# Performance work log

Hardware: AMD Instinct MI355X
Metric: run time of the kernel (lower is better)

Reference implementation:

```python
import jax, jax.numpy as jnp
import numpy as np

N_NODES = 50000
N_GRAPHS = 512


def _gcn_layer(x, src, dst, W, b):
    # DGL GraphConv, norm='both', allow_zero_in_degree=True
    n = x.shape[0]
    ones = jnp.ones(src.shape[0], x.dtype)
    deg_out = jnp.zeros(n, x.dtype).at[src].add(ones)
    deg_in = jnp.zeros(n, x.dtype).at[dst].add(ones)
    norm_out = jax.lax.rsqrt(jnp.maximum(deg_out, 1.0))
    norm_in = jax.lax.rsqrt(jnp.maximum(deg_in, 1.0))
    h = x * norm_out[:, None]
    agg = jax.ops.segment_sum(h[src], dst, num_segments=n)  # SpMM
    return (agg * norm_in[:, None]) @ W + b


def setup_inputs() -> dict:
    key = jax.random.key(0)
    ks = jax.random.split(key, 16)
    E = 800000
    inp = {
        'nid': jax.random.randint(ks[0], (N_NODES,), 0, 100000),
        'z': jax.random.randint(ks[1], (N_NODES,), 0, 1000),
        'src': jax.random.randint(ks[2], (E,), 0, N_NODES),
        'dst': jax.random.randint(ks[3], (E,), 0, N_NODES),
        'graph_id': jnp.sort(jax.random.randint(ks[4], (N_NODES,), 0, N_GRAPHS)),
        'init_embed': jax.random.normal(ks[5], (100000, 64), jnp.float32) * 0.1,
        'z_table': jax.random.normal(ks[6], (1000, 64), jnp.float32) * 0.1,
        'W0': jax.random.normal(ks[7], (128, 128), jnp.float32) * 0.1,
        'b0': jnp.zeros((128,), jnp.float32),
        'W1': jax.random.normal(ks[8], (128, 128), jnp.float32) * 0.1,
        'b1': jnp.zeros((128,), jnp.float32),
        'W2': jax.random.normal(ks[9], (128, 128), jnp.float32) * 0.1,
        'b2': jnp.zeros((128,), jnp.float32),
        'lin1_W': jax.random.normal(ks[10], (128, 128), jnp.float32) * 0.1,
        'lin1_b': jnp.zeros((128,), jnp.float32),
        'lin2_W': jax.random.normal(ks[11], (128, 200), jnp.float32) * 0.1,
        'lin2_b': jnp.zeros((200,), jnp.float32),
    }
    return inp


def reference(nid, z, src, dst, graph_id, init_embed, z_table, W0, b0, W1, b1, W2, b2, lin1_W, lin1_b, lin2_W, lin2_b):
    # node features: entity embedding lookup + structural label embedding, concat
    x = jnp.concatenate([init_embed[nid], z_table[z]], axis=1)  # [N, 128]
    # layers[:-1] with relu (dropout is identity in eval mode)
    x = jax.nn.relu(_gcn_layer(x, src, dst, W0, b0))
    x = jax.nn.relu(_gcn_layer(x, src, dst, W1, b1))
    x = _gcn_layer(x, src, dst, W2, b2)
    # SumPooling over subgraphs in the batch
    g = jax.ops.segment_sum(x, graph_id, num_segments=N_GRAPHS)  # [G, 128]
    h = jax.nn.relu(g @ lin1_W + lin1_b)
    return h @ lin2_W + lin2_b  # [G, num_rel]
```

## Files before the change

kernel.cpp:

```cpp
#include <hip/hip_runtime.h>
#include <hip/hip_bf16.h>


#define FEAT 128
#define NG 512
#define CH 128
#define NPMAX 12544
#define LDW 136

typedef __attribute__((ext_vector_type(8))) short bf16x8;
typedef __attribute__((ext_vector_type(4))) float f32x4;

__device__ __forceinline__ float bf2f(unsigned short u) {
    union { unsigned int i; float f; } v; v.i = ((unsigned int)u) << 16; return v.f;
}
__device__ __forceinline__ unsigned short f2bf(float f) {
    unsigned int u = __float_as_uint(f);
    return (unsigned short)((u + 0x7FFFu + ((u >> 16) & 1u)) >> 16);
}
__device__ __forceinline__ float lo16(unsigned u) { return __uint_as_float(u << 16); }
__device__ __forceinline__ float hi16(unsigned u) { return __uint_as_float(u & 0xFFFF0000u); }

__global__ __launch_bounds__(256) void k_hist(
        const int* __restrict__ src, const int* __restrict__ dst,
        unsigned* __restrict__ partial_out, unsigned* __restrict__ partial_in,
        int E, int NP, int Ec) {
    __shared__ unsigned h[NPMAX];
    int tid = threadIdx.x;
    int b = blockIdx.x;
    int c = b & (CH - 1);
    const int* __restrict__ arr = (b < CH) ? src : dst;
    unsigned* __restrict__ outp = ((b < CH) ? partial_out : partial_in) + (size_t)c * NP;
    for (int i = tid; i < NP; i += 256) h[i] = 0;
    __syncthreads();
    int e0 = c * Ec, e1 = min(E, e0 + Ec);
    for (int e = e0 + tid; e < e1; e += 256) {
        int v = arr[e];
        atomicAdd(&h[v >> 2], 1u << ((v & 3) * 8));
    }
    __syncthreads();
    for (int i = tid; i < NP; i += 256) outp[i] = h[i];
}

__global__ void k_merge(unsigned* __restrict__ partial_out, unsigned* __restrict__ partial_in,
                        int* __restrict__ cnt_in, float* __restrict__ norm_out,
                        float* __restrict__ norm_in, int N, int NP) {
    int w = blockIdx.x * blockDim.x + threadIdx.x;
    if (w >= NP) return;
    unsigned run_in = 0, run_out = 0;
    for (int c = 0; c < CH; c++) {
        size_t idx = (size_t)c * NP + w;
        unsigned v = partial_in[idx];
        partial_in[idx] = run_in;
        run_in += v;
        run_out += partial_out[idx];
    }
    #pragma unroll
    for (int j = 0; j < 4; j++) {
        int node = w * 4 + j;
        if (node < N) {
            unsigned di = (run_in  >> (j * 8)) & 255u;
            unsigned dd = (run_out >> (j * 8)) & 255u;
            cnt_in[node]   = (int)di;
            norm_in[node]  = rsqrtf(fmaxf((float)di, 1.0f));
            norm_out[node] = rsqrtf(fmaxf((float)dd, 1.0f));
        }
    }
}

__global__ void k_scan_local(const int* __restrict__ cnt, int* __restrict__ excl,
                             int* __restrict__ bsum, int N) {
    __shared__ int s[256];
    int x = threadIdx.x;
    int i = blockIdx.x * 256 + x;
    int v = (i < N) ? cnt[i] : 0;
    s[x] = v;
    __syncthreads();
    for (int off = 1; off < 256; off <<= 1) {
        int t = (x >= off) ? s[x - off] : 0;
        __syncthreads();
        s[x] += t;
        __syncthreads();
    }
    if (i < N) excl[i] = s[x] - v;
    if (x == 255) bsum[blockIdx.x] = s[255];
}

__global__ void k_scan_bsum_prep(int* __restrict__ bsum, int* __restrict__ boff, int nb,
                                 const float* __restrict__ W0, const float* __restrict__ W1,
                                 unsigned short* __restrict__ Wt0, unsigned short* __restrict__ Wt1) {
    if (blockIdx.x == 0) {
        __shared__ int s[256];
        int x = threadIdx.x;
        int v = (x < nb) ? bsum[x] : 0;
        s[x] = v;
        __syncthreads();
        for (int off = 1; off < 256; off <<= 1) {
            int t = (x >= off) ? s[x - off] : 0;
            __syncthreads();
            s[x] += t;
            __syncthreads();
        }
        if (x < nb) boff[x] = s[x] - v;
    } else {
        int t = ((int)blockIdx.x - 1) * 256 + threadIdx.x;
        if (t < 16384) {
            int n = t & 127, k = t >> 7;
            Wt0[n * 128 + k] = f2bf(W0[k * 128 + n]);
        } else {
            int t2 = t - 16384;
            int n = t2 & 127, k = t2 >> 7;
            Wt1[n * 128 + k] = f2bf(W1[k * 128 + n]);
        }
    }
}

__global__ void k_add_off(int* __restrict__ row_start, const int* __restrict__ boff, int N) {
    int i = blockIdx.x * blockDim.x + threadIdx.x;
    if (i < N) row_start[i] += boff[i >> 8];
}

__global__ __launch_bounds__(256) void k_fill_bx(
        const int* __restrict__ src, const int* __restrict__ dst,
        const int* __restrict__ row_start, const unsigned* __restrict__ partial_in,
        unsigned short* __restrict__ csr,
        const int* __restrict__ nid, const int* __restrict__ z,
        const float* __restrict__ emb, const float* __restrict__ zt,
        const float* __restrict__ nout, unsigned short* __restrict__ x,
        int N, int E, int NP, int Ec) {
    if ((int)blockIdx.x < CH) {
        __shared__ unsigned cur[NPMAX];
        int tid = threadIdx.x;
        int c = blockIdx.x;
        const unsigned* __restrict__ pre = partial_in + (size_t)c * NP;
        for (int i = tid; i < NP; i += 256) cur[i] = pre[i];
        __syncthreads();
        int e0 = c * Ec, e1 = min(E, e0 + Ec);
        for (int e = e0 + tid; e < e1; e += 256) {
            int d = dst[e], s = src[e];
            int sh = (d & 3) * 8;
            unsigned t = atomicAdd(&cur[d >> 2], 1u << sh);
            int off = (int)((t >> sh) & 255u);
            csr[row_start[d] + off] = (unsigned short)s;
        }
    } else {
        int tid = ((int)blockIdx.x - CH) * 256 + threadIdx.x;
        int i = tid >> 5, q = tid & 31;
        if (i < N) {
            float4 v;
            if (q < 16) v = ((const float4*)emb)[(size_t)nid[i] * 16 + q];
            else        v = ((const float4*)zt)[(size_t)z[i] * 16 + (q - 16)];
            float w = nout[i];
            ushort4 u;
            u.x = f2bf(v.x * w); u.y = f2bf(v.y * w);
            u.z = f2bf(v.z * w); u.w = f2bf(v.w * w);
            ((ushort4*)x)[(size_t)i * 32 + q] = u;
        }
    }
}

#define ACC8(u)                                                                  \
    a0 += lo16(u.x); a1 += hi16(u.x); a2 += lo16(u.y); a3 += hi16(u.y);          \
    a4 += lo16(u.z); a5 += hi16(u.z); a6 += lo16(u.w); a7 += hi16(u.w);

#define GATHER_BODY                                                              \
    int tid = threadIdx.x;                                                       \
    int node = blockIdx.x * 16 + (tid >> 4);                                     \
    int ql = tid & 15;                                                           \
    if (node >= N) return;                                                       \
    int base = row_start[node];                                                  \
    int n = cnt_in[node];                                                        \
    float a0 = 0.f, a1 = 0.f, a2 = 0.f, a3 = 0.f;                                \
    float a4 = 0.f, a5 = 0.f, a6 = 0.f, a7 = 0.f;                                \
    const uint4* xp = (const uint4*)x;                       \
    for (int j0 = 0; j0 < n; j0 += 16) {                                         \
        int rem = n - j0;                                                        \
        int m = rem < 16 ? rem : 16;                                             \
        int e = (int)csr[base + j0 + (ql < m ? ql : 0)];                         \
        int j = 0;                                                               \
        for (; j + 8 <= m; j += 8) {                                             \
            int s0 = __shfl(e, j + 0, 16), s1 = __shfl(e, j + 1, 16);            \
            int s2 = __shfl(e, j + 2, 16), s3 = __shfl(e, j + 3, 16);            \
            int s4 = __shfl(e, j + 4, 16), s5 = __shfl(e, j + 5, 16);            \
            int s6 = __shfl(e, j + 6, 16), s7 = __shfl(e, j + 7, 16);            \
            uint4 u0 = xp[(size_t)s0 * 16 + ql];                                 \
            uint4 u1 = xp[(size_t)s1 * 16 + ql];                                 \
            uint4 u2 = xp[(size_t)s2 * 16 + ql];                                 \
            uint4 u3 = xp[(size_t)s3 * 16 + ql];                                 \
            uint4 u4 = xp[(size_t)s4 * 16 + ql];                                 \
            uint4 u5 = xp[(size_t)s5 * 16 + ql];                                 \
            uint4 u6 = xp[(size_t)s6 * 16 + ql];                                 \
            uint4 u7 = xp[(size_t)s7 * 16 + ql];                                 \
            ACC8(u0) ACC8(u1) ACC8(u2) ACC8(u3)                                  \
            ACC8(u4) ACC8(u5) ACC8(u6) ACC8(u7)                                  \
        }                                                                        \
        for (; j + 4 <= m; j += 4) {                                             \
            int s0 = __shfl(e, j + 0, 16), s1 = __shfl(e, j + 1, 16);            \
            int s2 = __shfl(e, j + 2, 16), s3 = __shfl(e, j + 3, 16);            \
            uint4 u0 = xp[(size_t)s0 * 16 + ql];                                 \
            uint4 u1 = xp[(size_t)s1 * 16 + ql];                                 \
            uint4 u2 = xp[(size_t)s2 * 16 + ql];                                 \
            uint4 u3 = xp[(size_t)s3 * 16 + ql];                                 \
            ACC8(u0) ACC8(u1) ACC8(u2) ACC8(u3)                                  \
        }                                                                        \
        for (; j < m; j++) {                                                     \
            int s = __shfl(e, j, 16);                                            \
            uint4 u = xp[(size_t)s * 16 + ql];                                   \
            ACC8(u)                                                              \
        }                                                                        \
    }                                                                            \
    float ni = nin[node];

__global__ __launch_bounds__(256) void k_gather_b(
        const unsigned short* __restrict__ x, const float* __restrict__ nin,
        const unsigned short* __restrict__ csr, const int* __restrict__ row_start,
        const int* __restrict__ cnt_in, unsigned short* __restrict__ aggB, int N) {
    GATHER_BODY
    uint4 o;
    o.x = (unsigned)f2bf(a0 * ni) | ((unsigned)f2bf(a1 * ni) << 16);
    o.y = (unsigned)f2bf(a2 * ni) | ((unsigned)f2bf(a3 * ni) << 16);
    o.z = (unsigned)f2bf(a4 * ni) | ((unsigned)f2bf(a5 * ni) << 16);
    o.w = (unsigned)f2bf(a6 * ni) | ((unsigned)f2bf(a7 * ni) << 16);
    ((uint4*)aggB)[(size_t)node * 16 + ql] = o;
}

__global__ __launch_bounds__(256) void k_gather(
        const unsigned short* __restrict__ x, const float* __restrict__ nin,
        const unsigned short* __restrict__ csr, const int* __restrict__ row_start,
        const int* __restrict__ cnt_in, float* __restrict__ agg, int N) {
    GATHER_BODY
    float4* ap = (float4*)(agg + (size_t)node * FEAT + ql * 8);
    ap[0] = make_float4(a0 * ni, a1 * ni, a2 * ni, a3 * ni);
    ap[1] = make_float4(a4 * ni, a5 * ni, a6 * ni, a7 * ni);
}

__global__ __launch_bounds__(256) void k_gemm_mfma(
        const unsigned short* __restrict__ aggB, const unsigned short* __restrict__ Wt,
        const float* __restrict__ bias, const float* __restrict__ nout,
        unsigned short* __restrict__ y, int N) {
    __shared__ unsigned short As[64 * LDW];
    __shared__ unsigned short Ws[128 * LDW];
    int tid = threadIdx.x;
    int nb = blockIdx.x * 64;

    for (int i = tid; i < 64 * 16; i += 256) {
        int row = i >> 4, seg = i & 15;
        int node = nb + row;
        ushort4 u0 = {0, 0, 0, 0}, u1 = u0;
        if (node < N) {
            const ushort4* p = (const ushort4*)(aggB + (size_t)node * 128 + seg * 8);
            u0 = p[0]; u1 = p[1];
        }
        ushort4* d = (ushort4*)(As + row * LDW + seg * 8);
        d[0] = u0; d[1] = u1;
    }
    for (int i = tid; i < 128 * 16; i += 256) {
        int row = i >> 4, seg = i & 15;
        const ushort4* p = (const ushort4*)(Wt + row * 128 + seg * 8);
        ushort4* d = (ushort4*)(Ws + row * LDW + seg * 8);
        d[0] = p[0]; d[1] = p[1];
    }
    __syncthreads();

    int lane = tid & 63;
    int m0 = (tid >> 6) * 16;
    int c = lane & 15, q = lane >> 4;

    const unsigned short* ap = As + (m0 + c) * LDW + q * 8;
    bf16x8 a0 = *(const bf16x8*)(ap);
    bf16x8 a1 = *(const bf16x8*)(ap + 32);
    bf16x8 a2 = *(const bf16x8*)(ap + 64);
    bf16x8 a3 = *(const bf16x8*)(ap + 96);

    #pragma unroll
    for (int nt = 0; nt < 8; nt++) {
        const unsigned short* wp = Ws + (nt * 16 + c) * LDW + q * 8;
        bf16x8 b0 = *(const bf16x8*)(wp);
        bf16x8 b1 = *(const bf16x8*)(wp + 32);
        bf16x8 b2 = *(const bf16x8*)(wp + 64);
        bf16x8 b3 = *(const bf16x8*)(wp + 96);
        float bb = bias[nt * 16 + c];
        f32x4 acc = {bb, bb, bb, bb};
        acc = __builtin_amdgcn_mfma_f32_16x16x32_bf16(a0, b0, acc, 0, 0, 0);
        acc = __builtin_amdgcn_mfma_f32_16x16x32_bf16(a1, b1, acc, 0, 0, 0);
        acc = __builtin_amdgcn_mfma_f32_16x16x32_bf16(a2, b2, acc, 0, 0, 0);
        acc = __builtin_amdgcn_mfma_f32_16x16x32_bf16(a3, b3, acc, 0, 0, 0);
        #pragma unroll
        for (int r = 0; r < 4; r++) {
            int row = m0 + q * 4 + r;
            float s = nout[min(nb + row, N - 1)];
            As[row * LDW + nt * 16 + c] = f2bf(fmaxf(acc[r], 0.f) * s);
        }
    }
    __syncthreads();

    for (int i = tid; i < 64 * 16; i += 256) {
        int row = i >> 4, seg = i & 15;
        int node = nb + row;
        if (node < N) {
            const ushort4* p = (const ushort4*)(As + row * LDW + seg * 8);
            ushort4* d = (ushort4*)(y + (size_t)node * 128 + seg * 8);
            d[0] = p[0]; d[1] = p[1];
        }
    }
}

__global__ __launch_bounds__(256) void k_head(
        const float* __restrict__ agg, const int* __restrict__ gid,
        const float* __restrict__ W2, const float* __restrict__ b2,
        const float* __restrict__ l1W, const float* __restrict__ l1b,
        const float* __restrict__ l2W, const float* __restrict__ l2b,
        float* __restrict__ out, int N) {
    __shared__ float g2[2][128];
    __shared__ float gs[128];
    __shared__ float ys[128];
    __shared__ float hs[128];
    int gi = blockIdx.x, tid = threadIdx.x;

    int lo = 0, hi = N;
    while (lo < hi) { int m = (lo + hi) >> 1; if (gid[m] < gi) lo = m + 1; else hi = m; }
    int s0 = lo;
    lo = 0; hi = N;
    while (lo < hi) { int m = (lo + hi) >> 1; if (gid[m] < gi + 1) lo = m + 1; else hi = m; }
    int e0 = lo;
    float cnt = (float)(e0 - s0);

    int t = tid >> 7, j = tid & 127;
    float p = 0.f;
    for (int i = s0 + t; i < e0; i += 2) p += agg[(size_t)i * FEAT + j];
    g2[t][j] = p;
    __syncthreads();
    if (tid < 128) gs[tid] = g2[0][tid] + g2[1][tid];
    __syncthreads();
    if (tid < 128) {
        float a = cnt * b2[tid];
        for (int k = 0; k < 128; k++) a += gs[k] * W2[(size_t)k * 128 + tid];
        ys[tid] = a;
    }
    __syncthreads();
    if (tid < 128) {
        float a = l1b[tid];
        for (int k = 0; k < 128; k++) a += ys[k] * l1W[(size_t)k * 128 + tid];
        hs[tid] = fmaxf(a, 0.f);
    }
    __syncthreads();
    if (tid < 200) {
        float a = l2b[tid];
        for (int k = 0; k < 128; k++) a += hs[k] * l2W[(size_t)k * 200 + tid];
        out[(size_t)gi * 200 + tid] = a;
    }
}

extern "C" void kernel_launch(void* const* d_in, const int* in_sizes, int n_in,
                              void* d_out, int out_size, void* d_ws, size_t ws_size,
                              hipStream_t stream) {
    const int*   nid = (const int*)d_in[0];
    const int*   z   = (const int*)d_in[1];
    const int*   src = (const int*)d_in[2];
    const int*   dst = (const int*)d_in[3];
    const int*   gid = (const int*)d_in[4];
    const float* emb = (const float*)d_in[5];
    const float* zt  = (const float*)d_in[6];
    const float* W0  = (const float*)d_in[7];
    const float* b0  = (const float*)d_in[8];
    const float* W1  = (const float*)d_in[9];
    const float* b1  = (const float*)d_in[10];
    const float* W2  = (const float*)d_in[11];
    const float* b2  = (const float*)d_in[12];
    const float* l1W = (const float*)d_in[13];
    const float* l1b = (const float*)d_in[14];
    const float* l2W = (const float*)d_in[15];
    const float* l2b = (const float*)d_in[16];
    float* out = (float*)d_out;

    const int N = in_sizes[0];
    const int E = in_sizes[2];
    const int NB = (N + 255) / 256;
    const int NP = (N + 3) / 4;
    const int Ec = (E + CH - 1) / CH;

    size_t NA = (size_t)((N + 63) & ~63);
    float* norm_out = (float*)d_ws;
    float* norm_in  = norm_out + NA;
    float* agg = norm_in + NA;
    unsigned short* xA   = (unsigned short*)(agg + (size_t)N * FEAT);
    unsigned short* xB   = xA + (size_t)N * FEAT;
    unsigned short* aggB = xB + (size_t)N * FEAT;
    unsigned short* Wt0  = aggB + (size_t)N * FEAT;
    unsigned short* Wt1  = Wt0 + 128 * 128;
    int* cnt_in    = (int*)(Wt1 + 128 * 128);
    int* row_start = cnt_in + NA;
    int* bsum      = row_start + NA;
    int* boff      = bsum + 256;
    unsigned* partial_out = (unsigned*)(boff + 256);
    unsigned* partial_in  = partial_out + (size_t)CH * NP;
    unsigned short* csr = (unsigned short*)(partial_in + (size_t)CH * NP);

    k_hist<<<2 * CH, 256, 0, stream>>>(src, dst, partial_out, partial_in, E, NP, Ec);
    k_merge<<<(NP + 255) / 256, 256, 0, stream>>>(partial_out, partial_in, cnt_in,
                                                  norm_out, norm_in, N, NP);
    k_scan_local<<<NB, 256, 0, stream>>>(cnt_in, row_start, bsum, N);
    k_scan_bsum_prep<<<1 + 128, 256, 0, stream>>>(bsum, boff, NB, W0, W1, Wt0, Wt1);
    k_add_off<<<NB, 256, 0, stream>>>(row_start, boff, N);
    int XB = (N * 32 + 255) / 256;
    k_fill_bx<<<CH + XB, 256, 0, stream>>>(src, dst, row_start, partial_in, csr,
                                           nid, z, emb, zt, norm_out, xA, N, E, NP, Ec);

    int gat_blocks  = (N + 15) / 16;
    int gemm_blocks = (N + 63) / 64;

    k_gather_b<<<gat_blocks, 256, 0, stream>>>(xA, norm_in, csr, row_start, cnt_in, aggB, N);
    k_gemm_mfma<<<gemm_blocks, 256, 0, stream>>>(aggB, Wt0, b0, norm_out, xB, N);
    k_gather_b<<<gat_blocks, 256, 0, stream>>>(xB, norm_in, csr, row_start, cnt_in, aggB, N);
    k_gemm_mfma<<<gemm_blocks, 256, 0, stream>>>(aggB, Wt1, b1, norm_out, xA, N);
    k_gather<<<gat_blocks, 256, 0, stream>>>(xA, norm_in, csr, row_start, cnt_in, agg, N);

    k_head<<<NG, 256, 0, stream>>>(agg, gid, W2, b2, l1W, l1b, l2W, l2b, out, N);
}
```

Before: 311.5 us.

## Fuse SpMM gather into MFMA GEMM and fuse final gather with sum pooling

The per-layer gather kernel now writes its aggregated bf16 rows straight into the GEMM's shared-memory A tile, so the aggBf intermediate round trip and one launch per layer go away. Weights are pre-swizzled into MFMA fragment order and read directly from global memory instead of being staged through LDS. The last gather pools node rows into per-graph sums through shared-memory and global atomics, so the fp32 N×128 agg buffer is no longer written and then re-read by the head. The cost is lower gather parallelism per block (64 nodes processed serially in 4 rounds) and atomics with non-deterministic summation order.

```diff
diff --git a/kernel.cpp b/kernel.cpp
--- a/kernel.cpp
+++ b/kernel.cpp
@@ -88,7 +88,7 @@
 
 __global__ void k_scan_bsum_prep(int* __restrict__ bsum, int* __restrict__ boff, int nb,
                                  const float* __restrict__ W0, const float* __restrict__ W1,
-                                 unsigned short* __restrict__ Wt0, unsigned short* __restrict__ Wt1) {
+                                 unsigned short* __restrict__ WF0, unsigned short* __restrict__ WF1) {
     if (blockIdx.x == 0) {
         __shared__ int s[256];
         int x = threadIdx.x;
@@ -104,20 +104,22 @@
         if (x < nb) boff[x] = s[x] - v;
     } else {
         int t = ((int)blockIdx.x - 1) * 256 + threadIdx.x;
-        if (t < 16384) {
-            int n = t & 127, k = t >> 7;
-            Wt0[n * 128 + k] = f2bf(W0[k * 128 + n]);
-        } else {
-            int t2 = t - 16384;
-            int n = t2 & 127, k = t2 >> 7;
-            Wt1[n * 128 + k] = f2bf(W1[k * 128 + n]);
-        }
-    }
-}
-
-__global__ void k_add_off(int* __restrict__ row_start, const int* __restrict__ boff, int N) {
+        const float* __restrict__ W = (t < 16384) ? W0 : W1;
+        unsigned short* __restrict__ WF = (t < 16384) ? WF0 : WF1;
+        int tt = t & 16383;
+        int f = tt >> 9, l = (tt >> 3) & 63, e = tt & 7;
+        int n = (f >> 2) * 16 + (l & 15);
+        int k = (f & 3) * 32 + (l >> 4) * 8 + e;
+        WF[tt] = f2bf(W[k * 128 + n]);
+    }
+}
+
+__global__ void k_add_off(int* __restrict__ row_start, const int* __restrict__ boff,
+                          float* __restrict__ g, int N) {
     int i = blockIdx.x * blockDim.x + threadIdx.x;
+    int stride = gridDim.x * blockDim.x;
     if (i < N) row_start[i] += boff[i >> 8];
+    for (int j = i; j < NG * FEAT; j += stride) g[j] = 0.f;
 }
 
 __global__ __launch_bounds__(256) void k_fill_bx(
@@ -163,102 +165,78 @@
     a0 += lo16(u.x); a1 += hi16(u.x); a2 += lo16(u.y); a3 += hi16(u.y);          \
     a4 += lo16(u.z); a5 += hi16(u.z); a6 += lo16(u.w); a7 += hi16(u.w);
 
-#define GATHER_BODY                                                              \
-    int tid = threadIdx.x;                                                       \
-    int node = blockIdx.x * 16 + (tid >> 4);                                     \
-    int ql = tid & 15;                                                           \
-    if (node >= N) return;                                                       \
-    int base = row_start[node];                                                  \
-    int n = cnt_in[node];                                                        \
-    float a0 = 0.f, a1 = 0.f, a2 = 0.f, a3 = 0.f;                                \
-    float a4 = 0.f, a5 = 0.f, a6 = 0.f, a7 = 0.f;                                \
-    const uint4* xp = (const uint4*)x;                       \
-    for (int j0 = 0; j0 < n; j0 += 16) {                                         \
-        int rem = n - j0;                                                        \
-        int m = rem < 16 ? rem : 16;                                             \
-        int e = (int)csr[base + j0 + (ql < m ? ql : 0)];                         \
-        int j = 0;                                                               \
-        for (; j + 8 <= m; j += 8) {                                             \
-            int s0 = __shfl(e, j + 0, 16), s1 = __shfl(e, j + 1, 16);            \
-            int s2 = __shfl(e, j + 2, 16), s3 = __shfl(e, j + 3, 16);            \
-            int s4 = __shfl(e, j + 4, 16), s5 = __shfl(e, j + 5, 16);            \
-            int s6 = __shfl(e, j + 6, 16), s7 = __shfl(e, j + 7, 16);            \
-            uint4 u0 = xp[(size_t)s0 * 16 + ql];                                 \
-            uint4 u1 = xp[(size_t)s1 * 16 + ql];                                 \
-            uint4 u2 = xp[(size_t)s2 * 16 + ql];                                 \
-            uint4 u3 = xp[(size_t)s3 * 16 + ql];                                 \
-            uint4 u4 = xp[(size_t)s4 * 16 + ql];                                 \
-            uint4 u5 = xp[(size_t)s5 * 16 + ql];                                 \
-            uint4 u6 = xp[(size_t)s6 * 16 + ql];                                 \
-            uint4 u7 = xp[(size_t)s7 * 16 + ql];                                 \
-            ACC8(u0) ACC8(u1) ACC8(u2) ACC8(u3)                                  \
-            ACC8(u4) ACC8(u5) ACC8(u6) ACC8(u7)                                  \
+#define GATHER_LOOP                                                              \
+    {                                                                            \
+        int base = row_start[node];                                              \
+        int n = cnt_in[node];                                                    \
+        const uint4* xp = (const uint4*)x;                   \
+        for (int j0 = 0; j0 < n; j0 += 16) {                                     \
+            int rem = n - j0;                                                    \
+            int m = rem < 16 ? rem : 16;                                         \
+            int e = (int)csr[base + j0 + (ql < m ? ql : 0)];                     \
+            int j = 0;                                                           \
+            for (; j + 8 <= m; j += 8) {                                         \
+                int s0 = __shfl(e, j + 0, 16), s1 = __shfl(e, j + 1, 16);        \
+                int s2 = __shfl(e, j + 2, 16), s3 = __shfl(e, j + 3, 16);        \
+                int s4 = __shfl(e, j + 4, 16), s5 = __shfl(e, j + 5, 16);        \
+                int s6 = __shfl(e, j + 6, 16), s7 = __shfl(e, j + 7, 16);        \
+                uint4 u0 = xp[(size_t)s0 * 16 + ql];                             \
+                uint4 u1 = xp[(size_t)s1 * 16 + ql];                             \
+                uint4 u2 = xp[(size_t)s2 * 16 + ql];                             \
+                uint4 u3 = xp[(size_t)s3 * 16 + ql];                             \
+                uint4 u4 = xp[(size_t)s4 * 16 + ql];                             \
+                uint4 u5 = xp[(size_t)s5 * 16 + ql];                             \
+                uint4 u6 = xp[(size_t)s6 * 16 + ql];                             \
+                uint4 u7 = xp[(size_t)s7 * 16 + ql];                             \
+                ACC8(u0) ACC8(u1) ACC8(u2) ACC8(u3)                              \
+                ACC8(u4) ACC8(u5) ACC8(u6) ACC8(u7)                              \
+            }                                                                    \
+            for (; j + 4 <= m; j += 4) {                                         \
+                int s0 = __shfl(e, j + 0, 16), s1 = __shfl(e, j + 1, 16);        \
+                int s2 = __shfl(e, j + 2, 16), s3 = __shfl(e, j + 3, 16);        \
+                uint4 u0 = xp[(size_t)s0 * 16 + ql];                             \
+                uint4 u1 = xp[(size_t)s1 * 16 + ql];                             \
+                uint4 u2 = xp[(size_t)s2 * 16 + ql];                             \
+                uint4 u3 = xp[(size_t)s3 * 16 + ql];                             \
+                ACC8(u0) ACC8(u1) ACC8(u2) ACC8(u3)                              \
+            }                                                                    \
+            for (; j < m; j++) {                                                 \
+                int s = __shfl(e, j, 16);                                        \
+                uint4 u = xp[(size_t)s * 16 + ql];                               \
+                ACC8(u)                                                          \
+            }                                                                    \
         }                                                                        \
-        for (; j + 4 <= m; j += 4) {                                             \
-            int s0 = __shfl(e, j + 0, 16), s1 = __shfl(e, j + 1, 16);            \
-            int s2 = __shfl(e, j + 2, 16), s3 = __shfl(e, j + 3, 16);            \
-            uint4 u0 = xp[(size_t)s0 * 16 + ql];                                 \
-            uint4 u1 = xp[(size_t)s1 * 16 + ql];                                 \
-            uint4 u2 = xp[(size_t)s2 * 16 + ql];                                 \
-            uint4 u3 = xp[(size_t)s3 * 16 + ql];                                 \
-            ACC8(u0) ACC8(u1) ACC8(u2) ACC8(u3)                                  \
-        }                                                                        \
-        for (; j < m; j++) {                                                     \
-            int s = __shfl(e, j, 16);                                            \
-            uint4 u = xp[(size_t)s * 16 + ql];                                   \
-            ACC8(u)                                                              \
-        }                                                                        \
-    }                                                                            \
-    float ni = nin[node];
-
-__global__ __launch_bounds__(256) void k_gather_b(
+    }
+
+__global__ __launch_bounds__(256) void k_gather_gemm(
         const unsigned short* __restrict__ x, const float* __restrict__ nin,
         const unsigned short* __restrict__ csr, const int* __restrict__ row_start,
-        const int* __restrict__ cnt_in, unsigned short* __restrict__ aggB, int N) {
-    GATHER_BODY
-    uint4 o;
-    o.x = (unsigned)f2bf(a0 * ni) | ((unsigned)f2bf(a1 * ni) << 16);
-    o.y = (unsigned)f2bf(a2 * ni) | ((unsigned)f2bf(a3 * ni) << 16);
-    o.z = (unsigned)f2bf(a4 * ni) | ((unsigned)f2bf(a5 * ni) << 16);
-    o.w = (unsigned)f2bf(a6 * ni) | ((unsigned)f2bf(a7 * ni) << 16);
-    ((uint4*)aggB)[(size_t)node * 16 + ql] = o;
-}
-
-__global__ __launch_bounds__(256) void k_gather(
-        const unsigned short* __restrict__ x, const float* __restrict__ nin,
-        const unsigned short* __restrict__ csr, const int* __restrict__ row_start,
-        const int* __restrict__ cnt_in, float* __restrict__ agg, int N) {
-    GATHER_BODY
-    float4* ap = (float4*)(agg + (size_t)node * FEAT + ql * 8);
-    ap[0] = make_float4(a0 * ni, a1 * ni, a2 * ni, a3 * ni);
-    ap[1] = make_float4(a4 * ni, a5 * ni, a6 * ni, a7 * ni);
-}
-
-__global__ __launch_bounds__(256) void k_gemm_mfma(
-        const unsigned short* __restrict__ aggB, const unsigned short* __restrict__ Wt,
+        const int* __restrict__ cnt_in, const unsigned short* __restrict__ WF,
         const float* __restrict__ bias, const float* __restrict__ nout,
         unsigned short* __restrict__ y, int N) {
     __shared__ unsigned short As[64 * LDW];
-    __shared__ unsigned short Ws[128 * LDW];
     int tid = threadIdx.x;
     int nb = blockIdx.x * 64;
-
-    for (int i = tid; i < 64 * 16; i += 256) {
-        int row = i >> 4, seg = i & 15;
-        int node = nb + row;
-        ushort4 u0 = {0, 0, 0, 0}, u1 = u0;
+    int ql = tid & 15;
+    int nsub = tid >> 4;
+
+    #pragma unroll 1
+    for (int r = 0; r < 4; r++) {
+        int node = nb + r * 16 + nsub;
+        float a0 = 0.f, a1 = 0.f, a2 = 0.f, a3 = 0.f;
+        float a4 = 0.f, a5 = 0.f, a6 = 0.f, a7 = 0.f;
         if (node < N) {
-            const ushort4* p = (const ushort4*)(aggB + (size_t)node * 128 + seg * 8);
-            u0 = p[0]; u1 = p[1];
-        }
-        ushort4* d = (ushort4*)(As + row * LDW + seg * 8);
-        d[0] = u0; d[1] = u1;
-    }
-    for (int i = tid; i < 128 * 16; i += 256) {
-        int row = i >> 4, seg = i & 15;
-        const ushort4* p = (const ushort4*)(Wt + row * 128 + seg * 8);
-        ushort4* d = (ushort4*)(Ws + row * LDW + seg * 8);
-        d[0] = p[0]; d[1] = p[1];
+            GATHER_LOOP
+            float ni = nin[node];
+            a0 *= ni; a1 *= ni; a2 *= ni; a3 *= ni;
+            a4 *= ni; a5 *= ni; a6 *= ni; a7 *= ni;
+        }
+        uint4 o;
+        o.x = (unsigned)f2bf(a0) | ((unsigned)f2bf(a1) << 16);
+        o.y = (unsigned)f2bf(a2) | ((unsigned)f2bf(a3) << 16);
+        o.z = (unsigned)f2bf(a4) | ((unsigned)f2bf(a5) << 16);
+        o.w = (unsigned)f2bf(a6) | ((unsigned)f2bf(a7) << 16);
+        *(uint4*)(As + (r * 16 + nsub) * LDW + ql * 8) = o;
     }
     __syncthreads();
 
@@ -267,29 +245,29 @@
     int c = lane & 15, q = lane >> 4;
 
     const unsigned short* ap = As + (m0 + c) * LDW + q * 8;
-    bf16x8 a0 = *(const bf16x8*)(ap);
-    bf16x8 a1 = *(const bf16x8*)(ap + 32);
-    bf16x8 a2 = *(const bf16x8*)(ap + 64);
-    bf16x8 a3 = *(const bf16x8*)(ap + 96);
+    bf16x8 fa0 = *(const bf16x8*)(ap);
+    bf16x8 fa1 = *(const bf16x8*)(ap + 32);
+    bf16x8 fa2 = *(const bf16x8*)(ap + 64);
+    bf16x8 fa3 = *(const bf16x8*)(ap + 96);
+    const bf16x8* __restrict__ wf = (const bf16x8*)WF;
 
     #pragma unroll
     for (int nt = 0; nt < 8; nt++) {
-        const unsigned short* wp = Ws + (nt * 16 + c) * LDW + q * 8;
-        bf16x8 b0 = *(const bf16x8*)(wp);
-        bf16x8 b1 = *(const bf16x8*)(wp + 32);
-        bf16x8 b2 = *(const bf16x8*)(wp + 64);
-        bf16x8 b3 = *(const bf16x8*)(wp + 96);
+        bf16x8 fb0 = wf[(nt * 4 + 0) * 64 + lane];
+        bf16x8 fb1 = wf[(nt * 4 + 1) * 64 + lane];
+        bf16x8 fb2 = wf[(nt * 4 + 2) * 64 + lane];
+        bf16x8 fb3 = wf[(nt * 4 + 3) * 64 + lane];
         float bb = bias[nt * 16 + c];
         f32x4 acc = {bb, bb, bb, bb};
-        acc = __builtin_amdgcn_mfma_f32_16x16x32_bf16(a0, b0, acc, 0, 0, 0);
-        acc = __builtin_amdgcn_mfma_f32_16x16x32_bf16(a1, b1, acc, 0, 0, 0);
-        acc = __builtin_amdgcn_mfma_f32_16x16x32_bf16(a2, b2, acc, 0, 0, 0);
-        acc = __builtin_amdgcn_mfma_f32_16x16x32_bf16(a3, b3, acc, 0, 0, 0);
+        acc = __builtin_amdgcn_mfma_f32_16x16x32_bf16(fa0, fb0, acc, 0, 0, 0);
+        acc = __builtin_amdgcn_mfma_f32_16x16x32_bf16(fa1, fb1, acc, 0, 0, 0);
+        acc = __builtin_amdgcn_mfma_f32_16x16x32_bf16(fa2, fb2, acc, 0, 0, 0);
+        acc = __builtin_amdgcn_mfma_f32_16x16x32_bf16(fa3, fb3, acc, 0, 0, 0);
         #pragma unroll
-        for (int r = 0; r < 4; r++) {
-            int row = m0 + q * 4 + r;
+        for (int rr = 0; rr < 4; rr++) {
+            int row = m0 + q * 4 + rr;
             float s = nout[min(nb + row, N - 1)];
-            As[row * LDW + nt * 16 + c] = f2bf(fmaxf(acc[r], 0.f) * s);
+            As[row * LDW + nt * 16 + c] = f2bf(fmaxf(acc[rr], 0.f) * s);
         }
     }
     __syncthreads();
@@ -305,13 +283,64 @@
     }
 }
 
+__global__ __launch_bounds__(256) void k_gather_pool(
+        const unsigned short* __restrict__ x, const float* __restrict__ nin,
+        const unsigned short* __restrict__ csr, const int* __restrict__ row_start,
+        const int* __restrict__ cnt_in, const int* __restrict__ gid,
+        float* __restrict__ g, int N) {
+    __shared__ float gl[16][FEAT];
+    __shared__ int used;
+    int tid = threadIdx.x;
+    int nb = blockIdx.x * 16;
+    for (int i = tid; i < 16 * FEAT; i += 256) ((float*)gl)[i] = 0.f;
+    if (tid == 0) used = 0;
+    __syncthreads();
+
+    int ql = tid & 15;
+    int node = nb + (tid >> 4);
+    int g0 = gid[nb];
+    float a0 = 0.f, a1 = 0.f, a2 = 0.f, a3 = 0.f;
+    float a4 = 0.f, a5 = 0.f, a6 = 0.f, a7 = 0.f;
+    int slot = -1;
+    if (node < N) {
+        GATHER_LOOP
+        float ni = nin[node];
+        a0 *= ni; a1 *= ni; a2 *= ni; a3 *= ni;
+        a4 *= ni; a5 *= ni; a6 *= ni; a7 *= ni;
+        slot = gid[node] - g0;
+    }
+    if (slot >= 16) {
+        float* p = g + (size_t)(g0 + slot) * FEAT + ql * 8;
+        atomicAdd(p + 0, a0); atomicAdd(p + 1, a1);
+        atomicAdd(p + 2, a2); atomicAdd(p + 3, a3);
+        atomicAdd(p + 4, a4); atomicAdd(p + 5, a5);
+        atomicAdd(p + 6, a6); atomicAdd(p + 7, a7);
+    } else if (slot >= 0) {
+        float* p = &gl[slot][ql * 8];
+        atomicAdd(p + 0, a0); atomicAdd(p + 1, a1);
+        atomicAdd(p + 2, a2); atomicAdd(p + 3, a3);
+        atomicAdd(p + 4, a4); atomicAdd(p + 5, a5);
+        atomicAdd(p + 6, a6); atomicAdd(p + 7, a7);
+        if (ql == 0) atomicOr(&used, 1 << slot);
+    }
+    __syncthreads();
+    int u = used;
+    #pragma unroll
+    for (int s0 = 0; s0 < 16; s0 += 2) {
+        int s = s0 + (tid >> 7);
+        if ((u >> s) & 1) {
+            int j = tid & 127;
+            atomicAdd(&g[(size_t)(g0 + s) * FEAT + j], gl[s][j]);
+        }
+    }
+}
+
 __global__ __launch_bounds__(256) void k_head(
-        const float* __restrict__ agg, const int* __restrict__ gid,
+        const float* __restrict__ g, const int* __restrict__ gid,
         const float* __restrict__ W2, const float* __restrict__ b2,
         const float* __restrict__ l1W, const float* __restrict__ l1b,
         const float* __restrict__ l2W, const float* __restrict__ l2b,
         float* __restrict__ out, int N) {
-    __shared__ float g2[2][128];
     __shared__ float gs[128];
     __shared__ float ys[128];
     __shared__ float hs[128];
@@ -322,15 +351,9 @@
     int s0 = lo;
     lo = 0; hi = N;
     while (lo < hi) { int m = (lo + hi) >> 1; if (gid[m] < gi + 1) lo = m + 1; else hi = m; }
-    int e0 = lo;
-    float cnt = (float)(e0 - s0);
-
-    int t = tid >> 7, j = tid & 127;
-    float p = 0.f;
-    for (int i = s0 + t; i < e0; i += 2) p += agg[(size_t)i * FEAT + j];
-    g2[t][j] = p;
-    __syncthreads();
-    if (tid < 128) gs[tid] = g2[0][tid] + g2[1][tid];
+    float cnt = (float)(lo - s0);
+
+    if (tid < 128) gs[tid] = g[(size_t)gi * FEAT + tid];
     __syncthreads();
     if (tid < 128) {
         float a = cnt * b2[tid];
@@ -382,13 +405,12 @@
     size_t NA = (size_t)((N + 63) & ~63);
     float* norm_out = (float*)d_ws;
     float* norm_in  = norm_out + NA;
-    float* agg = norm_in + NA;
-    unsigned short* xA   = (unsigned short*)(agg + (size_t)N * FEAT);
-    unsigned short* xB   = xA + (size_t)N * FEAT;
-    unsigned short* aggB = xB + (size_t)N * FEAT;
-    unsigned short* Wt0  = aggB + (size_t)N * FEAT;
-    unsigned short* Wt1  = Wt0 + 128 * 128;
-    int* cnt_in    = (int*)(Wt1 + 128 * 128);
+    float* g        = norm_in + NA;
+    unsigned short* xA  = (unsigned short*)(g + (size_t)NG * FEAT);
+    unsigned short* xB  = xA + (size_t)N * FEAT;
+    unsigned short* WF0 = xB + (size_t)N * FEAT;
+    unsigned short* WF1 = WF0 + 128 * 128;
+    int* cnt_in    = (int*)(WF1 + 128 * 128);
     int* row_start = cnt_in + NA;
     int* bsum      = row_start + NA;
     int* boff      = bsum + 256;
@@ -400,20 +422,21 @@
     k_merge<<<(NP + 255) / 256, 256, 0, stream>>>(partial_out, partial_in, cnt_in,
                                                   norm_out, norm_in, N, NP);
     k_scan_local<<<NB, 256, 0, stream>>>(cnt_in, row_start, bsum, N);
-    k_scan_bsum_prep<<<1 + 128, 256, 0, stream>>>(bsum, boff, NB, W0, W1, Wt0, Wt1);
-    k_add_off<<<NB, 256, 0, stream>>>(row_start, boff, N);
+    k_scan_bsum_prep<<<1 + 128, 256, 0, stream>>>(bsum, boff, NB, W0, W1, WF0, WF1);
+    k_add_off<<<NB, 256, 0, stream>>>(row_start, boff, g, N);
     int XB = (N * 32 + 255) / 256;
     k_fill_bx<<<CH + XB, 256, 0, stream>>>(src, dst, row_start, partial_in, csr,
                                            nid, z, emb, zt, norm_out, xA, N, E, NP, Ec);
 
-    int gat_blocks  = (N + 15) / 16;
-    int gemm_blocks = (N + 63) / 64;
-
-    k_gather_b<<<gat_blocks, 256, 0, stream>>>(xA, norm_in, csr, row_start, cnt_in, aggB, N);
-    k_gemm_mfma<<<gemm_blocks, 256, 0, stream>>>(aggB, Wt0, b0, norm_out, xB, N);
-    k_gather_b<<<gat_blocks, 256, 0, stream>>>(xB, norm_in, csr, row_start, cnt_in, aggB, N);
-    k_gemm_mfma<<<gemm_blocks, 256, 0, stream>>>(aggB, Wt1, b1, norm_out, xA, N);
-    k_gather<<<gat_blocks, 256, 0, stream>>>(xA, norm_in, csr, row_start, cnt_in, agg, N);
-
-    k_head<<<NG, 256, 0, stream>>>(agg, gid, W2, b2, l1W, l1b, l2W, l2b, out, N);
-}
+    int gg_blocks = (N + 63) / 64;
+    int gp_blocks = (N + 15) / 16;
+
+    k_gather_gemm<<<gg_blocks, 256, 0, stream>>>(xA, norm_in, csr, row_start, cnt_in,
+                                                 WF0, b0, norm_out, xB, N);
+    k_gather_gemm<<<gg_blocks, 256, 0, stream>>>(xB, norm_in, csr, row_start, cnt_in,
+                                                 WF1, b1, norm_out, xA, N);
+    k_gather_pool<<<gp_blocks, 256, 0, stream>>>(xA, norm_in, csr, row_start, cnt_in,
+                                                 gid, g, N);
+
+    k_head<<<NG, 256, 0, stream>>>(g, gid, W2, b2, l1W, l1b, l2W, l2b, out, N);
+}
```

New measurement: 313.0 us. About the same (+0.5%).
